# Kernel tuning notes

Measured on AMD Instinct MI355X. Metric: run time of the kernel, lower is better.

## Reference

```python
import jax, jax.numpy as jnp
import numpy as np

# Fixed tetrahedral (kanchor=4) rotation->anchor permutation table, taken verbatim
# from the docstring in the original source (trace_idx_ori).
TRACE_IDX_ORI = jnp.array([
    [0, 1, 2, 3], [0, 2, 3, 1], [0, 3, 1, 2],
    [1, 2, 0, 3], [1, 0, 3, 2], [1, 3, 2, 0],
    [2, 3, 0, 1], [2, 0, 1, 3], [2, 1, 3, 0],
    [3, 1, 0, 2], [3, 0, 2, 1], [3, 2, 1, 0]], dtype=jnp.int32)

B, A, N, M, D, H = 1, 4, 384, 384, 256, 8
C = D // H  # d_model_per_head = 32
NR = TRACE_IDX_ORI.shape[0]  # 12 rotations


def _project_heads(x, W, b):
    # x: (b, a, n, d) -> (b, a, h, n, c)
    y = x @ W.T + b
    bb, aa, nn, _ = y.shape
    return y.reshape(bb, aa, nn, H, C).transpose(0, 1, 3, 2, 4)


def setup_inputs() -> dict:
    key = jax.random.key(0)
    ks = jax.random.split(key, 6)
    s = 1.0 / np.sqrt(D).astype(np.float32)
    return {
        "input_q": jax.random.normal(ks[0], (B, A, N, D), dtype=jnp.float32),
        "input_k": jax.random.normal(ks[1], (B, A, M, D), dtype=jnp.float32),
        "input_v": jax.random.normal(ks[2], (B, A, M, D), dtype=jnp.float32),
        "Wq": jax.random.normal(ks[3], (D, D), dtype=jnp.float32) * s,
        "bq": jnp.zeros((D,), dtype=jnp.float32),
        "Wk": jax.random.normal(ks[4], (D, D), dtype=jnp.float32) * s,
        "bk": jnp.zeros((D,), dtype=jnp.float32),
        "Wv": jax.random.normal(ks[5], (D, D), dtype=jnp.float32) * s,
        "bv": jnp.zeros((D,), dtype=jnp.float32),
    }


def reference(input_q, input_k, input_v, Wq, bq, Wk, bk, Wv, bv):
    # Step 0: linear projections + split heads.  q,k,v: (b, a, h, n|m, c)
    q = _project_heads(input_q, Wq, bq)
    k = _project_heads(input_k, Wk, bk)
    v = _project_heads(input_v, Wv, bv)

    # Step 1: per-anchor-pair local attention scores: (b, a, e, h, n, m)
    scores_ae = jnp.einsum('bahnc,behmc->baehnm', q, k) / jnp.sqrt(
        jnp.asarray(C, dtype=q.dtype))

    # Step 2: rotation-wise gather (attn_mode='r_soft', alternative_impl=False).
    # For rotation r, query anchor a attends to key anchor trace_idx_ori[r, a]:
    # scores_rot[b, r, a] = scores_ae[b, a, trace_idx_ori[r, a]]  -> (b, nr, a, h, n, m)
    a_idx = jnp.arange(A, dtype=jnp.int32)[None, :]  # (1, A) broadcasts vs (NR, A)
    scores_rot = scores_ae[:, a_idx, TRACE_IDX_ORI]

    # Global rotation attention: pool over anchors/heads/points (attn_r_summ='mean',
    # attn_r_multihead=False), make non-negative ('sq'), normalize over rotations.
    pooled = jnp.mean(scores_rot, axis=(2, 3, 4, 5))  # (b, nr)
    pos = pooled * pooled
    attn_r = pos / jnp.sum(pos, axis=-1, keepdims=True)  # (b, nr)

    # Step 3+4: softmax over key points per rotation, gather values per rotation,
    # then weight by the global rotation attention.
    attn_local = jax.nn.softmax(scores_rot, axis=-1)  # (b, nr, a, h, n, m)
    v_rot = v[:, TRACE_IDX_ORI]  # (b, nr, a, h, m, c)
    hidden = jnp.einsum('br,brahnm,brahmc->bahnc', attn_r, attn_local, v_rot)

    # Merge heads: (b, a, h, n, c) -> (b, a, n, h*c)
    out = hidden.transpose(0, 1, 3, 2, 4).reshape(B, A, N, D)
    return out
```

## Files before the change

### kernel.cpp

```cpp
#include <hip/hip_runtime.h>
#include <hip/hip_bf16.h>

typedef __attribute__((ext_vector_type(8))) short s8x8;
typedef __attribute__((ext_vector_type(4))) float f32x4;

__device__ __forceinline__ ushort f2bf(float x) {
    union { float f; unsigned u; } c; c.f = x;
    unsigned r = c.u + 0x7FFFu + ((c.u >> 16) & 1u);
    return (ushort)(r >> 16);
}
__device__ __forceinline__ float bf2f(ushort b) {
    union { unsigned u; float f; } c; c.u = ((unsigned)b) << 16;
    return c.f;
}

__global__ __launch_bounds__(256) void proj_kernel(
    const float* __restrict__ Xq, const float* __restrict__ Xk,
    const float* __restrict__ Xv,
    const float* __restrict__ Wq, const float* __restrict__ bq,
    const float* __restrict__ Wk, const float* __restrict__ bk,
    const float* __restrict__ Wv, const float* __restrict__ bv,
    ushort* __restrict__ qh, ushort* __restrict__ ql,
    ushort* __restrict__ kh, ushort* __restrict__ kl,
    ushort* __restrict__ vh)
{
    const int z = blockIdx.z;
    const float* X    = (z == 0) ? Xq : (z == 1) ? Xk : Xv;
    const float* W    = (z == 0) ? Wq : (z == 1) ? Wk : Wv;
    const float* bias = (z == 0) ? bq : (z == 1) ? bk : bv;

    __shared__ float Xs[64][17];
    __shared__ float Ws[64][17];
    __shared__ float T[64][65];

    const int tid = threadIdx.x;
    const int row0 = blockIdx.x * 64;
    const int col0 = blockIdx.y * 64;
    const int tx = tid & 15;
    const int ty = tid >> 4;

    float acc[4][4];
    #pragma unroll
    for (int i = 0; i < 4; ++i)
        #pragma unroll
        for (int j = 0; j < 4; ++j) acc[i][j] = 0.f;

    for (int kt = 0; kt < 256; kt += 16) {
        const int r  = tid >> 2;
        const int k4 = (tid & 3) * 4;
        float4 xv = *(const float4*)&X[(row0 + r) * 256 + kt + k4];
        Xs[r][k4 + 0] = xv.x; Xs[r][k4 + 1] = xv.y;
        Xs[r][k4 + 2] = xv.z; Xs[r][k4 + 3] = xv.w;
        float4 wv = *(const float4*)&W[(col0 + r) * 256 + kt + k4];
        Ws[r][k4 + 0] = wv.x; Ws[r][k4 + 1] = wv.y;
        Ws[r][k4 + 2] = wv.z; Ws[r][k4 + 3] = wv.w;
        __syncthreads();
        #pragma unroll
        for (int kk = 0; kk < 16; ++kk) {
            float xr[4], wc[4];
            #pragma unroll
            for (int i = 0; i < 4; ++i) xr[i] = Xs[ty + 16 * i][kk];
            #pragma unroll
            for (int j = 0; j < 4; ++j) wc[j] = Ws[tx + 16 * j][kk];
            #pragma unroll
            for (int i = 0; i < 4; ++i)
                #pragma unroll
                for (int j = 0; j < 4; ++j) acc[i][j] += xr[i] * wc[j];
        }
        __syncthreads();
    }

    if (z != 2) {
        #pragma unroll
        for (int i = 0; i < 4; ++i) {
            const int row = row0 + ty + 16 * i;
            const int ae = row / 384;
            const int n = row - ae * 384;
            #pragma unroll
            for (int j = 0; j < 4; ++j) {
                const int d = col0 + tx + 16 * j;
                const int hd = d >> 5;
                const int c = d & 31;
                const float v = acc[i][j] + bias[d];
                const ushort hb = f2bf(v);
                const ushort lb = f2bf(v - bf2f(hb));
                if (z == 0) {
                    const size_t idx = ((size_t)((ae * 8 + hd) * 384 + n)) * 32 + c;
                    qh[idx] = hb; ql[idx] = lb;
                } else {
                    const size_t idx =
                        ((size_t)(((ae * 8 + hd) * 4 + (c >> 3)) * 384 + n)) * 8 + (c & 7);
                    kh[idx] = hb; kl[idx] = lb;
                }
            }
        }
    } else {
        #pragma unroll
        for (int i = 0; i < 4; ++i)
            #pragma unroll
            for (int j = 0; j < 4; ++j)
                T[ty + 16 * i][tx + 16 * j] = acc[i][j] + bias[col0 + tx + 16 * j];
        __syncthreads();
        const int cc_l = tid >> 2;
        const int nb = (tid & 3) * 16;
        const int d = col0 + cc_l;
        const int hd = d >> 5;
        const int c = d & 31;
        const int ae = row0 / 384;
        const int e8h = ae * 8 + hd;
        ushort hbuf[16] __attribute__((aligned(16)));
        #pragma unroll
        for (int k16 = 0; k16 < 16; ++k16)
            hbuf[k16] = f2bf(T[nb + k16][cc_l]);
        const size_t base = (size_t)(e8h * 32 + c) * 384 + (row0 % 384) + nb;
        *(uint4*)&vh[base] = *(const uint4*)&hbuf[0];
        *(uint4*)&vh[base + 8] = *(const uint4*)&hbuf[8];
    }
}

__global__ __launch_bounds__(192) void attn_mfma_kernel(
    const ushort* __restrict__ qhb, const ushort* __restrict__ qlb,
    const ushort* __restrict__ khb, const ushort* __restrict__ klb,
    const ushort* __restrict__ vhb,
    float* __restrict__ Sout, float* __restrict__ msum_part)
{
    __shared__ ushort Kh[4 * 192 * 8];
    __shared__ ushort Kl[4 * 192 * 8];
    __shared__ ushort Vh[32 * 200];
    __shared__ float  Pl[3][2][16][36];
    __shared__ float  red[192];

    const int strip = blockIdx.x;
    const int aeh   = blockIdx.y;
    const int hh    = aeh & 7;
    const int ee    = (aeh >> 3) & 3;
    const int aa    = aeh >> 5;
    const int e8h   = ee * 8 + hh;
    const int a8h   = aa * 8 + hh;
    const int tid   = threadIdx.x;
    const int wave  = tid >> 6;
    const int lane  = tid & 63;
    const int lg    = lane >> 4;
    const int ll    = lane & 15;

    s8x8 qfh[2], qfl[2];
    #pragma unroll
    for (int r = 0; r < 2; ++r) {
        const int n0 = strip * 96 + (2 * wave + r) * 16;
        const size_t off = (size_t)(a8h * 384 + n0 + ll) * 32 + lg * 8;
        qfh[r] = *(const s8x8*)&qhb[off];
        qfl[r] = *(const s8x8*)&qlb[off];
    }

    f32x4 oacc[2][2];
    #pragma unroll
    for (int r = 0; r < 2; ++r)
        #pragma unroll
        for (int ct = 0; ct < 2; ++ct)
            oacc[r][ct] = (f32x4){0.f, 0.f, 0.f, 0.f};
    float lsum[2][4];
    #pragma unroll
    for (int r = 0; r < 2; ++r)
        #pragma unroll
        for (int j = 0; j < 4; ++j) lsum[r][j] = 0.f;
    float rs = 0.f;
    const float sc = 0.17677669529663687f;

    for (int half = 0; half < 2; ++half) {
        #pragma unroll
        for (int i = 0; i < 4; ++i) {
            const size_t src = ((size_t)(e8h * 4 + i) * 384 + half * 192 + tid) * 8;
            *(uint4*)&Kh[(i * 192 + tid) * 8] = *(const uint4*)&khb[src];
            *(uint4*)&Kl[(i * 192 + tid) * 8] = *(const uint4*)&klb[src];
        }
        #pragma unroll
        for (int i = 0; i < 4; ++i) {
            const int u = tid + 192 * i;
            const int c = u / 24;
            const int m8 = (u - c * 24) * 8;
            *(uint4*)&Vh[c * 200 + m8] =
                *(const uint4*)&vhb[(size_t)(e8h * 32 + c) * 384 + half * 192 + m8];
        }
        __syncthreads();

        for (int mt2 = 0; mt2 < 6; ++mt2) {
            #pragma unroll
            for (int sub = 0; sub < 2; ++sub) {
                const int mt = mt2 * 2 + sub;
                const s8x8 kfh = *(const s8x8*)&Kh[(lg * 192 + mt * 16 + ll) * 8];
                const s8x8 kfl = *(const s8x8*)&Kl[(lg * 192 + mt * 16 + ll) * 8];
                #pragma unroll
                for (int r = 0; r < 2; ++r) {
                    f32x4 s = {0.f, 0.f, 0.f, 0.f};
                    s = __builtin_amdgcn_mfma_f32_16x16x32_bf16(qfh[r], kfh, s, 0, 0, 0);
                    s = __builtin_amdgcn_mfma_f32_16x16x32_bf16(qfl[r], kfh, s, 0, 0, 0);
                    s = __builtin_amdgcn_mfma_f32_16x16x32_bf16(qfh[r], kfl, s, 0, 0, 0);
                    rs += s[0] + s[1] + s[2] + s[3];
                    #pragma unroll
                    for (int j = 0; j < 4; ++j) {
                        const float p = __expf(s[j] * sc);
                        lsum[r][j] += p;
                        Pl[wave][r][lg * 4 + j][sub * 16 + ll] = p;
                    }
                }
            }
            const int mloc = mt2 * 32;
            const s8x8 vf0 = *(const s8x8*)&Vh[(0  + ll) * 200 + mloc + lg * 8];
            const s8x8 vf1 = *(const s8x8*)&Vh[(16 + ll) * 200 + mloc + lg * 8];
            #pragma unroll
            for (int r = 0; r < 2; ++r) {
                const float* prow = &Pl[wave][r][ll][lg * 8];
                s8x8 pah, pal;
                #pragma unroll
                for (int e2 = 0; e2 < 8; ++e2) {
                    const float pv = prow[e2];
                    const ushort hb = f2bf(pv);
                    pah[e2] = (short)hb;
                    pal[e2] = (short)f2bf(pv - bf2f(hb));
                }
                oacc[r][0] = __builtin_amdgcn_mfma_f32_16x16x32_bf16(pah, vf0, oacc[r][0], 0, 0, 0);
                oacc[r][0] = __builtin_amdgcn_mfma_f32_16x16x32_bf16(pal, vf0, oacc[r][0], 0, 0, 0);
                oacc[r][1] = __builtin_amdgcn_mfma_f32_16x16x32_bf16(pah, vf1, oacc[r][1], 0, 0, 0);
                oacc[r][1] = __builtin_amdgcn_mfma_f32_16x16x32_bf16(pal, vf1, oacc[r][1], 0, 0, 0);
            }
        }
        __syncthreads();
    }

    #pragma unroll
    for (int r = 0; r < 2; ++r) {
        #pragma unroll
        for (int j = 0; j < 4; ++j) {
            float L = lsum[r][j];
            L += __shfl_xor(L, 1);
            L += __shfl_xor(L, 2);
            L += __shfl_xor(L, 4);
            L += __shfl_xor(L, 8);
            const float invL = 1.f / L;
            const int row = strip * 96 + (2 * wave + r) * 16 + lg * 4 + j;
            const size_t base = (size_t)(aeh * 384 + row) * 32;
            Sout[base + 0  + ll] = oacc[r][0][j] * invL;
            Sout[base + 16 + ll] = oacc[r][1][j] * invL;
        }
    }

    red[tid] = rs * sc;
    __syncthreads();
    for (int off = 96; off >= 3; off >>= 1) {
        if (tid < off) red[tid] += red[tid + off];
        __syncthreads();
    }
    if (tid == 0) msum_part[aeh * 4 + strip] = red[0] + red[1] + red[2];
}

__global__ __launch_bounds__(256) void stats_kernel(
    const float* __restrict__ msum_part, float* __restrict__ wout)
{
    __shared__ float sh[128];
    __shared__ float cell[16];
    const int tid = threadIdx.x;
    if (tid < 128) {
        float s = 0.f;
        #pragma unroll
        for (int j = 0; j < 4; ++j) s += msum_part[tid * 4 + j];
        sh[tid] = s;
    }
    __syncthreads();
    if (tid < 16) {
        const int base = (tid >> 2) * 32 + (tid & 3) * 8;
        float s = 0.f;
        #pragma unroll
        for (int hh = 0; hh < 8; ++hh) s += sh[base + hh];
        cell[tid] = s;
    }
    __syncthreads();
    if (tid == 0) {
        const int TR[12][4] = {
            {0,1,2,3},{0,2,3,1},{0,3,1,2},{1,2,0,3},{1,0,3,2},{1,3,2,0},
            {2,3,0,1},{2,0,1,3},{2,1,3,0},{3,1,0,2},{3,0,2,1},{3,2,1,0}};
        const float denom = 4.0f * 8.0f * 384.0f * 384.0f;
        float pos[12];
        float psum = 0.f;
        for (int r = 0; r < 12; ++r) {
            float s = 0.f;
            for (int aa = 0; aa < 4; ++aa) s += cell[aa * 4 + TR[r][aa]];
            const float pooled = s / denom;
            pos[r] = pooled * pooled;
            psum += pos[r];
        }
        float w[16];
        for (int i = 0; i < 16; ++i) w[i] = 0.f;
        const float ip = 1.f / psum;
        for (int r = 0; r < 12; ++r)
            for (int aa = 0; aa < 4; ++aa) w[aa * 4 + TR[r][aa]] += pos[r] * ip;
        for (int i = 0; i < 16; ++i) wout[i] = w[i];
    }
}

__global__ __launch_bounds__(256) void combine_kernel(
    const float* __restrict__ S, const float* __restrict__ w,
    float* __restrict__ out)
{
    const int idx = blockIdx.x * 256 + threadIdx.x;
    const int a = idx / 98304;
    const int rem = idx - a * 98304;
    const int n = rem >> 8;
    const int d = rem & 255;
    const int h = d >> 5;
    const int c = d & 31;
    float r = 0.f;
    #pragma unroll
    for (int e = 0; e < 4; ++e)
        r += w[a * 4 + e] * S[(size_t)(((a * 4 + e) * 8 + h) * 384 + n) * 32 + c];
    out[idx] = r;
}

extern "C" void kernel_launch(void* const* d_in, const int* in_sizes, int n_in,
                              void* d_out, int out_size, void* d_ws, size_t ws_size,
                              hipStream_t stream)
{
    const float* in_q = (const float*)d_in[0];
    const float* in_k = (const float*)d_in[1];
    const float* in_v = (const float*)d_in[2];
    const float* Wq   = (const float*)d_in[3];
    const float* bq   = (const float*)d_in[4];
    const float* Wk   = (const float*)d_in[5];
    const float* bk   = (const float*)d_in[6];
    const float* Wv   = (const float*)d_in[7];
    const float* bv   = (const float*)d_in[8];

    const size_t NE = 393216;
    ushort* qh = (ushort*)d_ws;
    ushort* ql = qh + NE;
    ushort* kh = ql + NE;
    ushort* kl = kh + NE;
    ushort* vh = kl + NE;
    float*  Sb = (float*)((char*)d_ws + 5 * NE * sizeof(ushort));
    float*  ms = Sb + 1572864;
    float*  wb = ms + 512;
    float*  outp = (float*)d_out;

    dim3 pgrid(24, 4, 3);
    proj_kernel<<<pgrid, 256, 0, stream>>>(in_q, in_k, in_v, Wq, bq, Wk, bk,
                                           Wv, bv, qh, ql, kh, kl, vh);
    dim3 agrid(4, 128);
    attn_mfma_kernel<<<agrid, 192, 0, stream>>>(qh, ql, kh, kl, vh, Sb, ms);
    stats_kernel<<<1, 256, 0, stream>>>(ms, wb);
    combine_kernel<<<1536, 256, 0, stream>>>(Sb, wb, outp);
}
```

Measured before the change: 53.97 us.

## Use split-bf16 MFMA projection, bf16 P in attention, fuse stats into combine

Adds a prep kernel that splits X and W into hi/lo bf16 pairs, with W stored in an MFMA-friendly layout. The FP32 SIMT projection GEMM is replaced by a 3-term split-bf16 MFMA GEMM. In attention, probabilities are stored to LDS as single bf16 instead of fp32 re-split into hi/lo, which halves the PV MFMAs. It also pads the K LDS layout, adds s_setprio around MFMA blocks, and folds stats_kernel into a float4-vectorized combine kernel. The bf16-only P lowers precision of the softmax weights, and the extra prep pass adds a kernel launch and workspace traffic.

```diff
diff --git a/kernel.cpp b/kernel.cpp
--- a/kernel.cpp
+++ b/kernel.cpp
@@ -14,107 +14,148 @@
     return c.f;
 }
 
-__global__ __launch_bounds__(256) void proj_kernel(
+__global__ __launch_bounds__(256) void prep_kernel(
     const float* __restrict__ Xq, const float* __restrict__ Xk,
     const float* __restrict__ Xv,
-    const float* __restrict__ Wq, const float* __restrict__ bq,
-    const float* __restrict__ Wk, const float* __restrict__ bk,
-    const float* __restrict__ Wv, const float* __restrict__ bv,
+    const float* __restrict__ Wq, const float* __restrict__ Wk,
+    const float* __restrict__ Wv,
+    ushort* __restrict__ xh, ushort* __restrict__ xl,
+    ushort* __restrict__ wbh, ushort* __restrict__ wbl)
+{
+    const int id = blockIdx.x * 256 + threadIdx.x;
+    if (id < 294912) {
+        const int z = id / 98304;
+        const int r = id - z * 98304;
+        const float* X = (z == 0) ? Xq : (z == 1) ? Xk : Xv;
+        const float4 v = *(const float4*)&X[(size_t)r * 4];
+        const float vv[4] = {v.x, v.y, v.z, v.w};
+        unsigned h0 = 0, h1 = 0, l0 = 0, l1 = 0;
+        {
+            const ushort a0 = f2bf(vv[0]), a1 = f2bf(vv[1]);
+            const ushort a2 = f2bf(vv[2]), a3 = f2bf(vv[3]);
+            h0 = (unsigned)a0 | ((unsigned)a1 << 16);
+            h1 = (unsigned)a2 | ((unsigned)a3 << 16);
+            const ushort b0 = f2bf(vv[0] - bf2f(a0)), b1 = f2bf(vv[1] - bf2f(a1));
+            const ushort b2 = f2bf(vv[2] - bf2f(a2)), b3 = f2bf(vv[3] - bf2f(a3));
+            l0 = (unsigned)b0 | ((unsigned)b1 << 16);
+            l1 = (unsigned)b2 | ((unsigned)b3 << 16);
+        }
+        const size_t dst = (size_t)z * 393216 + (size_t)r * 4;
+        *(uint2*)&xh[dst] = make_uint2(h0, h1);
+        *(uint2*)&xl[dst] = make_uint2(l0, l1);
+    } else if (id < 344064) {
+        const int wid = id - 294912;
+        const int z = wid / 16384;
+        const int r = wid - z * 16384;
+        const int col = r >> 6;
+        const int k4 = (r & 63) * 4;
+        const float* W = (z == 0) ? Wq : (z == 1) ? Wk : Wv;
+        const float4 v = *(const float4*)&W[(size_t)col * 256 + k4];
+        const float vv[4] = {v.x, v.y, v.z, v.w};
+        const int kk = k4 >> 5;
+        const int lg = (k4 >> 3) & 3;
+        const int j0 = k4 & 7;
+        unsigned h0, h1, l0, l1;
+        {
+            const ushort a0 = f2bf(vv[0]), a1 = f2bf(vv[1]);
+            const ushort a2 = f2bf(vv[2]), a3 = f2bf(vv[3]);
+            h0 = (unsigned)a0 | ((unsigned)a1 << 16);
+            h1 = (unsigned)a2 | ((unsigned)a3 << 16);
+            const ushort b0 = f2bf(vv[0] - bf2f(a0)), b1 = f2bf(vv[1] - bf2f(a1));
+            const ushort b2 = f2bf(vv[2] - bf2f(a2)), b3 = f2bf(vv[3] - bf2f(a3));
+            l0 = (unsigned)b0 | ((unsigned)b1 << 16);
+            l1 = (unsigned)b2 | ((unsigned)b3 << 16);
+        }
+        const size_t dst = (size_t)z * 65536 + ((size_t)((kk * 4 + lg) * 256 + col)) * 8 + j0;
+        *(uint2*)&wbh[dst] = make_uint2(h0, h1);
+        *(uint2*)&wbl[dst] = make_uint2(l0, l1);
+    }
+}
+
+__global__ __launch_bounds__(256) void proj_kernel(
+    const ushort* __restrict__ xh, const ushort* __restrict__ xl,
+    const ushort* __restrict__ wbh, const ushort* __restrict__ wbl,
+    const float* __restrict__ bq, const float* __restrict__ bk,
+    const float* __restrict__ bv,
     ushort* __restrict__ qh, ushort* __restrict__ ql,
     ushort* __restrict__ kh, ushort* __restrict__ kl,
     ushort* __restrict__ vh)
 {
     const int z = blockIdx.z;
-    const float* X    = (z == 0) ? Xq : (z == 1) ? Xk : Xv;
-    const float* W    = (z == 0) ? Wq : (z == 1) ? Wk : Wv;
     const float* bias = (z == 0) ? bq : (z == 1) ? bk : bv;
-
-    __shared__ float Xs[64][17];
-    __shared__ float Ws[64][17];
-    __shared__ float T[64][65];
-
     const int tid = threadIdx.x;
-    const int row0 = blockIdx.x * 64;
-    const int col0 = blockIdx.y * 64;
-    const int tx = tid & 15;
-    const int ty = tid >> 4;
-
-    float acc[4][4];
-    #pragma unroll
-    for (int i = 0; i < 4; ++i)
-        #pragma unroll
-        for (int j = 0; j < 4; ++j) acc[i][j] = 0.f;
-
-    for (int kt = 0; kt < 256; kt += 16) {
-        const int r  = tid >> 2;
-        const int k4 = (tid & 3) * 4;
-        float4 xv = *(const float4*)&X[(row0 + r) * 256 + kt + k4];
-        Xs[r][k4 + 0] = xv.x; Xs[r][k4 + 1] = xv.y;
-        Xs[r][k4 + 2] = xv.z; Xs[r][k4 + 3] = xv.w;
-        float4 wv = *(const float4*)&W[(col0 + r) * 256 + kt + k4];
-        Ws[r][k4 + 0] = wv.x; Ws[r][k4 + 1] = wv.y;
-        Ws[r][k4 + 2] = wv.z; Ws[r][k4 + 3] = wv.w;
-        __syncthreads();
-        #pragma unroll
-        for (int kk = 0; kk < 16; ++kk) {
-            float xr[4], wc[4];
-            #pragma unroll
-            for (int i = 0; i < 4; ++i) xr[i] = Xs[ty + 16 * i][kk];
-            #pragma unroll
-            for (int j = 0; j < 4; ++j) wc[j] = Ws[tx + 16 * j][kk];
-            #pragma unroll
-            for (int i = 0; i < 4; ++i)
-                #pragma unroll
-                for (int j = 0; j < 4; ++j) acc[i][j] += xr[i] * wc[j];
-        }
-        __syncthreads();
-    }
+    const int wave = tid >> 6;
+    const int lane = tid & 63;
+    const int lg = lane >> 4;
+    const int ll = lane & 15;
+    const int bx = blockIdx.x;
+    const int by = blockIdx.y;
+
+    const ushort* xhz = xh + (size_t)z * 393216;
+    const ushort* xlz = xl + (size_t)z * 393216;
+    const ushort* wbhz = wbh + (size_t)z * 65536;
+    const ushort* wblz = wbl + (size_t)z * 65536;
+    const int rbase = bx * 64 + wave * 16;
+
+    f32x4 acc[4];
+    #pragma unroll
+    for (int ct = 0; ct < 4; ++ct) acc[ct] = (f32x4){0.f, 0.f, 0.f, 0.f};
+
+    #pragma unroll
+    for (int kk = 0; kk < 8; ++kk) {
+        const size_t aoff = (size_t)(rbase + ll) * 256 + kk * 32 + lg * 8;
+        const s8x8 axh = *(const s8x8*)&xhz[aoff];
+        const s8x8 axl = *(const s8x8*)&xlz[aoff];
+        #pragma unroll
+        for (int ct = 0; ct < 4; ++ct) {
+            const size_t boff = ((size_t)((kk * 4 + lg) * 256 + by * 64 + ct * 16 + ll)) * 8;
+            const s8x8 bh = *(const s8x8*)&wbhz[boff];
+            const s8x8 bl = *(const s8x8*)&wblz[boff];
+            acc[ct] = __builtin_amdgcn_mfma_f32_16x16x32_bf16(axh, bh, acc[ct], 0, 0, 0);
+            acc[ct] = __builtin_amdgcn_mfma_f32_16x16x32_bf16(axl, bh, acc[ct], 0, 0, 0);
+            acc[ct] = __builtin_amdgcn_mfma_f32_16x16x32_bf16(axh, bl, acc[ct], 0, 0, 0);
+        }
+    }
+
+    const int ae = bx / 6;
+    const int nbase = (bx - ae * 6) * 64 + wave * 16 + lg * 4;
 
     if (z != 2) {
         #pragma unroll
-        for (int i = 0; i < 4; ++i) {
-            const int row = row0 + ty + 16 * i;
-            const int ae = row / 384;
-            const int n = row - ae * 384;
+        for (int ct = 0; ct < 4; ++ct) {
+            const float bb = bias[by * 64 + ct * 16 + ll];
+            const int hsel = by * 2 + (ct >> 1);
+            const int csel = (ct & 1) * 16 + ll;
             #pragma unroll
             for (int j = 0; j < 4; ++j) {
-                const int d = col0 + tx + 16 * j;
-                const int hd = d >> 5;
-                const int c = d & 31;
-                const float v = acc[i][j] + bias[d];
+                const int n = nbase + j;
+                const float v = acc[ct][j] + bb;
                 const ushort hb = f2bf(v);
                 const ushort lb = f2bf(v - bf2f(hb));
                 if (z == 0) {
-                    const size_t idx = ((size_t)((ae * 8 + hd) * 384 + n)) * 32 + c;
+                    const size_t idx = ((size_t)((ae * 8 + hsel) * 384 + n)) * 32 + csel;
                     qh[idx] = hb; ql[idx] = lb;
                 } else {
                     const size_t idx =
-                        ((size_t)(((ae * 8 + hd) * 4 + (c >> 3)) * 384 + n)) * 8 + (c & 7);
+                        ((size_t)(((ae * 8 + hsel) * 4 + (csel >> 3)) * 384 + n)) * 8 + (csel & 7);
                     kh[idx] = hb; kl[idx] = lb;
                 }
             }
         }
     } else {
         #pragma unroll
-        for (int i = 0; i < 4; ++i)
+        for (int ct = 0; ct < 4; ++ct) {
+            const float bb = bias[by * 64 + ct * 16 + ll];
+            const int hsel = by * 2 + (ct >> 1);
+            const int csel = (ct & 1) * 16 + ll;
+            ushort p[4];
             #pragma unroll
-            for (int j = 0; j < 4; ++j)
-                T[ty + 16 * i][tx + 16 * j] = acc[i][j] + bias[col0 + tx + 16 * j];
-        __syncthreads();
-        const int cc_l = tid >> 2;
-        const int nb = (tid & 3) * 16;
-        const int d = col0 + cc_l;
-        const int hd = d >> 5;
-        const int c = d & 31;
-        const int ae = row0 / 384;
-        const int e8h = ae * 8 + hd;
-        ushort hbuf[16] __attribute__((aligned(16)));
-        #pragma unroll
-        for (int k16 = 0; k16 < 16; ++k16)
-            hbuf[k16] = f2bf(T[nb + k16][cc_l]);
-        const size_t base = (size_t)(e8h * 32 + c) * 384 + (row0 % 384) + nb;
-        *(uint4*)&vh[base] = *(const uint4*)&hbuf[0];
-        *(uint4*)&vh[base + 8] = *(const uint4*)&hbuf[8];
+            for (int j = 0; j < 4; ++j) p[j] = f2bf(acc[ct][j] + bb);
+            const unsigned u0 = (unsigned)p[0] | ((unsigned)p[1] << 16);
+            const unsigned u1 = (unsigned)p[2] | ((unsigned)p[3] << 16);
+            const size_t basei = ((size_t)((ae * 8 + hsel) * 32 + csel)) * 384 + nbase;
+            *(uint2*)&vh[basei] = make_uint2(u0, u1);
+        }
     }
 }
 
@@ -124,10 +165,10 @@
     const ushort* __restrict__ vhb,
     float* __restrict__ Sout, float* __restrict__ msum_part)
 {
-    __shared__ ushort Kh[4 * 192 * 8];
-    __shared__ ushort Kl[4 * 192 * 8];
+    __shared__ ushort Kh[4 * 1544];
+    __shared__ ushort Kl[4 * 1544];
     __shared__ ushort Vh[32 * 200];
-    __shared__ float  Pl[3][2][16][36];
+    __shared__ ushort Pl[3 * 2 * 16 * 40];
     __shared__ float  red[192];
 
     const int strip = blockIdx.x;
@@ -170,8 +211,8 @@
         #pragma unroll
         for (int i = 0; i < 4; ++i) {
             const size_t src = ((size_t)(e8h * 4 + i) * 384 + half * 192 + tid) * 8;
-            *(uint4*)&Kh[(i * 192 + tid) * 8] = *(const uint4*)&khb[src];
-            *(uint4*)&Kl[(i * 192 + tid) * 8] = *(const uint4*)&klb[src];
+            *(uint4*)&Kh[i * 1544 + tid * 8] = *(const uint4*)&khb[src];
+            *(uint4*)&Kl[i * 1544 + tid * 8] = *(const uint4*)&klb[src];
         }
         #pragma unroll
         for (int i = 0; i < 4; ++i) {
@@ -187,20 +228,22 @@
             #pragma unroll
             for (int sub = 0; sub < 2; ++sub) {
                 const int mt = mt2 * 2 + sub;
-                const s8x8 kfh = *(const s8x8*)&Kh[(lg * 192 + mt * 16 + ll) * 8];
-                const s8x8 kfl = *(const s8x8*)&Kl[(lg * 192 + mt * 16 + ll) * 8];
+                const s8x8 kfh = *(const s8x8*)&Kh[lg * 1544 + (mt * 16 + ll) * 8];
+                const s8x8 kfl = *(const s8x8*)&Kl[lg * 1544 + (mt * 16 + ll) * 8];
                 #pragma unroll
                 for (int r = 0; r < 2; ++r) {
                     f32x4 s = {0.f, 0.f, 0.f, 0.f};
+                    __builtin_amdgcn_s_setprio(1);
                     s = __builtin_amdgcn_mfma_f32_16x16x32_bf16(qfh[r], kfh, s, 0, 0, 0);
                     s = __builtin_amdgcn_mfma_f32_16x16x32_bf16(qfl[r], kfh, s, 0, 0, 0);
                     s = __builtin_amdgcn_mfma_f32_16x16x32_bf16(qfh[r], kfl, s, 0, 0, 0);
+                    __builtin_amdgcn_s_setprio(0);
                     rs += s[0] + s[1] + s[2] + s[3];
                     #pragma unroll
                     for (int j = 0; j < 4; ++j) {
                         const float p = __expf(s[j] * sc);
                         lsum[r][j] += p;
-                        Pl[wave][r][lg * 4 + j][sub * 16 + ll] = p;
+                        Pl[((wave * 2 + r) * 16 + lg * 4 + j) * 40 + sub * 16 + ll] = f2bf(p);
                     }
                 }
             }
@@ -209,19 +252,11 @@
             const s8x8 vf1 = *(const s8x8*)&Vh[(16 + ll) * 200 + mloc + lg * 8];
             #pragma unroll
             for (int r = 0; r < 2; ++r) {
-                const float* prow = &Pl[wave][r][ll][lg * 8];
-                s8x8 pah, pal;
-                #pragma unroll
-                for (int e2 = 0; e2 < 8; ++e2) {
-                    const float pv = prow[e2];
-                    const ushort hb = f2bf(pv);
-                    pah[e2] = (short)hb;
-                    pal[e2] = (short)f2bf(pv - bf2f(hb));
-                }
-                oacc[r][0] = __builtin_amdgcn_mfma_f32_16x16x32_bf16(pah, vf0, oacc[r][0], 0, 0, 0);
-                oacc[r][0] = __builtin_amdgcn_mfma_f32_16x16x32_bf16(pal, vf0, oacc[r][0], 0, 0, 0);
-                oacc[r][1] = __builtin_amdgcn_mfma_f32_16x16x32_bf16(pah, vf1, oacc[r][1], 0, 0, 0);
-                oacc[r][1] = __builtin_amdgcn_mfma_f32_16x16x32_bf16(pal, vf1, oacc[r][1], 0, 0, 0);
+                const s8x8 pa = *(const s8x8*)&Pl[((wave * 2 + r) * 16 + ll) * 40 + lg * 8];
+                __builtin_amdgcn_s_setprio(1);
+                oacc[r][0] = __builtin_amdgcn_mfma_f32_16x16x32_bf16(pa, vf0, oacc[r][0], 0, 0, 0);
+                oacc[r][1] = __builtin_amdgcn_mfma_f32_16x16x32_bf16(pa, vf1, oacc[r][1], 0, 0, 0);
+                __builtin_amdgcn_s_setprio(0);
             }
         }
         __syncthreads();
@@ -253,11 +288,13 @@
     if (tid == 0) msum_part[aeh * 4 + strip] = red[0] + red[1] + red[2];
 }
 
-__global__ __launch_bounds__(256) void stats_kernel(
-    const float* __restrict__ msum_part, float* __restrict__ wout)
+__global__ __launch_bounds__(256) void combine_kernel(
+    const float* __restrict__ S, const float* __restrict__ msum_part,
+    float* __restrict__ out)
 {
     __shared__ float sh[128];
     __shared__ float cell[16];
+    __shared__ float wsh[16];
     const int tid = threadIdx.x;
     if (tid < 128) {
         float s = 0.f;
@@ -270,7 +307,7 @@
         const int base = (tid >> 2) * 32 + (tid & 3) * 8;
         float s = 0.f;
         #pragma unroll
-        for (int hh = 0; hh < 8; ++hh) s += sh[base + hh];
+        for (int h2 = 0; h2 < 8; ++h2) s += sh[base + h2];
         cell[tid] = s;
     }
     __syncthreads();
@@ -283,7 +320,7 @@
         float psum = 0.f;
         for (int r = 0; r < 12; ++r) {
             float s = 0.f;
-            for (int aa = 0; aa < 4; ++aa) s += cell[aa * 4 + TR[r][aa]];
+            for (int a2 = 0; a2 < 4; ++a2) s += cell[a2 * 4 + TR[r][a2]];
             const float pooled = s / denom;
             pos[r] = pooled * pooled;
             psum += pos[r];
@@ -292,27 +329,26 @@
         for (int i = 0; i < 16; ++i) w[i] = 0.f;
         const float ip = 1.f / psum;
         for (int r = 0; r < 12; ++r)
-            for (int aa = 0; aa < 4; ++aa) w[aa * 4 + TR[r][aa]] += pos[r] * ip;
-        for (int i = 0; i < 16; ++i) wout[i] = w[i];
-    }
-}
-
-__global__ __launch_bounds__(256) void combine_kernel(
-    const float* __restrict__ S, const float* __restrict__ w,
-    float* __restrict__ out)
-{
-    const int idx = blockIdx.x * 256 + threadIdx.x;
-    const int a = idx / 98304;
-    const int rem = idx - a * 98304;
-    const int n = rem >> 8;
-    const int d = rem & 255;
-    const int h = d >> 5;
-    const int c = d & 31;
-    float r = 0.f;
-    #pragma unroll
-    for (int e = 0; e < 4; ++e)
-        r += w[a * 4 + e] * S[(size_t)(((a * 4 + e) * 8 + h) * 384 + n) * 32 + c];
-    out[idx] = r;
+            for (int a2 = 0; a2 < 4; ++a2) w[a2 * 4 + TR[r][a2]] += pos[r] * ip;
+        for (int i = 0; i < 16; ++i) wsh[i] = w[i];
+    }
+    __syncthreads();
+
+    const int idx4 = blockIdx.x * 256 + tid;
+    const int a = idx4 / 24576;
+    const int rem = idx4 - a * 24576;
+    const int n = rem >> 6;
+    const int d4 = rem & 63;
+    const int h = d4 >> 3;
+    const int c0 = (d4 & 7) * 4;
+    float4 r = make_float4(0.f, 0.f, 0.f, 0.f);
+    #pragma unroll
+    for (int e = 0; e < 4; ++e) {
+        const float wv = wsh[a * 4 + e];
+        const float4 s = *(const float4*)&S[(size_t)(((a * 4 + e) * 8 + h) * 384 + n) * 32 + c0];
+        r.x += wv * s.x; r.y += wv * s.y; r.z += wv * s.z; r.w += wv * s.w;
+    }
+    *(float4*)&out[(size_t)idx4 * 4] = r;
 }
 
 extern "C" void kernel_launch(void* const* d_in, const int* in_sizes, int n_in,
@@ -329,22 +365,27 @@
     const float* Wv   = (const float*)d_in[7];
     const float* bv   = (const float*)d_in[8];
 
-    const size_t NE = 393216;
-    ushort* qh = (ushort*)d_ws;
-    ushort* ql = qh + NE;
-    ushort* kh = ql + NE;
-    ushort* kl = kh + NE;
-    ushort* vh = kl + NE;
-    float*  Sb = (float*)((char*)d_ws + 5 * NE * sizeof(ushort));
-    float*  ms = Sb + 1572864;
-    float*  wb = ms + 512;
+    char* base = (char*)d_ws;
+    float*  Sb = (float*)base;
+    ushort* xh = (ushort*)base;
+    ushort* xl = xh + 1179648;
+    char* p2 = base + 6291456;
+    ushort* wbh = (ushort*)p2;
+    ushort* wbl = wbh + 196608;
+    ushort* qh  = wbl + 196608;
+    ushort* ql  = qh + 393216;
+    ushort* kh  = ql + 393216;
+    ushort* kl  = kh + 393216;
+    ushort* vh  = kl + 393216;
+    float*  ms  = (float*)(vh + 393216);
     float*  outp = (float*)d_out;
 
+    prep_kernel<<<1344, 256, 0, stream>>>(in_q, in_k, in_v, Wq, Wk, Wv,
+                                          xh, xl, wbh, wbl);
     dim3 pgrid(24, 4, 3);
-    proj_kernel<<<pgrid, 256, 0, stream>>>(in_q, in_k, in_v, Wq, bq, Wk, bk,
-                                           Wv, bv, qh, ql, kh, kl, vh);
+    proj_kernel<<<pgrid, 256, 0, stream>>>(xh, xl, wbh, wbl, bq, bk, bv,
+                                           qh, ql, kh, kl, vh);
     dim3 agrid(4, 128);
     attn_mfma_kernel<<<agrid, 192, 0, stream>>>(qh, ql, kh, kl, vh, Sb, ms);
-    stats_kernel<<<1, 256, 0, stream>>>(ms, wb);
-    combine_kernel<<<1536, 256, 0, stream>>>(Sb, wb, outp);
-}
+    combine_kernel<<<384, 256, 0, stream>>>(Sb, ms, outp);
+}
```

Result: faster. 49.35 us (-8.6%).
